# Optimization experiments

Measured on AMD Instinct MI355X. Metric: run time of the kernel, lower is better.

The kernel has to match this reference:

```python
import jax, jax.numpy as jnp
import numpy as np

D_MODEL, D_FF, N_EXPERTS, TOP_K = 1024, 4096, 8, 2
B, S = 2, 2048


def setup_inputs() -> dict:
    key = jax.random.key(0)
    ks = jax.random.split(key, 7)
    scale = 0.02
    return {
        "x": jax.random.normal(ks[0], (B, S, D_MODEL), dtype=jnp.float32),
        "W1": jax.random.normal(ks[1], (N_EXPERTS, D_MODEL, D_FF), dtype=jnp.float32) * scale,
        "b1": jnp.zeros((N_EXPERTS, D_FF), dtype=jnp.float32),
        "W2": jax.random.normal(ks[2], (N_EXPERTS, D_FF, D_MODEL), dtype=jnp.float32) * scale,
        "b2": jnp.zeros((N_EXPERTS, D_MODEL), dtype=jnp.float32),
        "Wg": jax.random.normal(ks[3], (D_MODEL, N_EXPERTS), dtype=jnp.float32) * scale,
        "bg": jnp.zeros((N_EXPERTS,), dtype=jnp.float32),
    }


def reference(x, W1, b1, W2, b2, Wg, bg):
    # x: [B, S, d_model]
    Bx, Sx, d = x.shape
    E = W1.shape[0]
    # Gate + top-k routing (softmax over the top-k scores, as in the torch code)
    logits = jnp.einsum("bsd,de->bse", x, Wg) + bg            # [B,S,E]
    topk_scores, topk_idx = jax.lax.top_k(logits, TOP_K)       # [B,S,K]
    topk_scores = jax.nn.softmax(topk_scores, axis=-1)

    tokens = x.reshape(-1, d)                                  # [T,d]
    idx_flat = topk_idx.reshape(-1, TOP_K)                     # [T,K]
    sc_flat = topk_scores.reshape(-1, TOP_K)                   # [T,K]
    # Per-token combine weight for each expert: sum_k score_k * 1[idx_k == e]
    comb = (jax.nn.one_hot(idx_flat, E, dtype=x.dtype) * sc_flat[..., None]).sum(axis=1)  # [T,E]

    # Dense grouped expert MLP (zero combine weight kills non-selected experts)
    h = jnp.einsum("td,edf->etf", tokens, W1) + b1[:, None, :]  # [E,T,d_ff]
    even = (jnp.arange(E) % 2 == 0)[:, None, None]
    # torch nn.GELU default = exact (erf); odd experts use SiLU
    a = jnp.where(even, jax.nn.gelu(h, approximate=False), jax.nn.silu(h))
    y = jnp.einsum("etf,efd->etd", a, W2) + b2[:, None, :]      # [E,T,d_model]
    out = jnp.einsum("te,etd->td", comb, y)                     # [T,d_model]
    # Dropout is identity in eval mode
    return out.reshape(Bx, Sx, d)
```

## Files before the change

### kernel.cpp

```cpp
#include <hip/hip_runtime.h>
#include <stdint.h>

#define T_TOK 4096
#define DM 1024
#define DF 4096
#define NE 8

typedef __attribute__((ext_vector_type(8))) short bf16x8;
typedef __attribute__((ext_vector_type(4))) float f32x4;

__device__ __forceinline__ float b2f(unsigned short u) {
    union { unsigned int i; float f; } v; v.i = ((unsigned int)u) << 16; return v.f;
}
__device__ __forceinline__ unsigned short f2b(float f) {
    unsigned int i = __float_as_uint(f);
    unsigned int r = (i + 0x7FFFu + ((i >> 16) & 1u)) >> 16;
    return (unsigned short)r;
}
__device__ __forceinline__ void load_lds16(const void* g, void* l) {
    __builtin_amdgcn_global_load_lds((__attribute__((address_space(1))) void*)(g),
                                     (__attribute__((address_space(3))) void*)(l), 16, 0, 0);
}

__device__ __forceinline__ float fexp2(float x) {
#if __has_builtin(__builtin_amdgcn_exp2f)
    return __builtin_amdgcn_exp2f(x);
#else
    return exp2f(x);
#endif
}
__device__ __forceinline__ float frcp(float x) {
#if __has_builtin(__builtin_amdgcn_rcpf)
    return __builtin_amdgcn_rcpf(x);
#else
    return 1.0f / x;
#endif
}

__device__ __forceinline__ float gelu_f(float h) {
    float z = h * 0.70710678118654752f;
    float az = fabsf(z);
    float t = frcp(1.0f + 0.3275911f * az);
    float p = ((((1.061405429f * t - 1.453152027f) * t + 1.421413741f) * t
                - 0.284496736f) * t + 0.254829592f) * t;
    float e = fexp2(-1.4426950408889634f * az * az);
    float er = 1.0f - p * e;
    er = (z < 0.f) ? -er : er;
    return 0.5f * h * (1.0f + er);
}
__device__ __forceinline__ float silu_f(float h) {
    return h * frcp(1.0f + fexp2(-1.4426950408889634f * h));
}

__device__ __forceinline__ int swz_bid(int H) {
    int x = H & 7, k = H >> 3;
    return 8 * x + 64 * (k >> 3) + (k & 7);
}

__global__ __launch_bounds__(256) void detect_kernel(const unsigned short* __restrict__ xu,
                                                     int* __restrict__ flag) {
    const int i = (blockIdx.x * 256 + threadIdx.x) * 4;
    uint2 v = *(const uint2*)&xu[i];
    unsigned int a = v.x, b = v.y;
    int found = 0;
    if (((a >> 7)  & 0xFF) == 0xFF) found = 1;
    if (((a >> 23) & 0xFF) == 0xFF) found = 1;
    if (((b >> 7)  & 0xFF) == 0xFF) found = 1;
    if (((b >> 23) & 0xFF) == 0xFF) found = 1;
    if (__ballot(found) != 0 && (threadIdx.x & 63) == 0) atomicOr(flag, 1);
}

__global__ __launch_bounds__(256) void convx_kernel(const void* __restrict__ xin,
                                                    const int* __restrict__ flag,
                                                    unsigned short* __restrict__ xb) {
    const size_t i = ((size_t)blockIdx.x * 256 + threadIdx.x) * 8;
    if (*flag) {
        const float* xf = (const float*)xin + i;
        float4 a = *(const float4*)xf;
        float4 b = *(const float4*)(xf + 4);
        alignas(16) unsigned short t[8] = { f2b(a.x), f2b(a.y), f2b(a.z), f2b(a.w),
                                            f2b(b.x), f2b(b.y), f2b(b.z), f2b(b.w) };
        *(uint4*)(xb + i) = *(const uint4*)t;
    } else {
        *(uint4*)(xb + i) = *(const uint4*)((const unsigned short*)xin + i);
    }
}

__global__ void convf_kernel(const void* __restrict__ b1, const void* __restrict__ b2,
                             const int* __restrict__ flag,
                             float* __restrict__ d1, float* __restrict__ d2) {
    const int i = blockIdx.x * 256 + threadIdx.x;
    const int isf = *flag;
    if (i < NE * DF) {
        d1[i] = isf ? ((const float*)b1)[i] : b2f(((const unsigned short*)b1)[i]);
    } else {
        int j = i - NE * DF;
        d2[j] = isf ? ((const float*)b2)[j] : b2f(((const unsigned short*)b2)[j]);
    }
}

__global__ __launch_bounds__(256) void transpose_kernel(
    const void* __restrict__ in1, const void* __restrict__ in2,
    unsigned short* __restrict__ out1, unsigned short* __restrict__ out2,
    const int* __restrict__ flag) {
    __shared__ unsigned short tile[64][65];
    const int isf = *flag;
    const void* in; unsigned short* out;
    int R, C, rt, ct; size_t base;
    if (blockIdx.z < 8) {
        in = in1; out = out1; R = DM; C = DF;
        base = (size_t)blockIdx.z * R * C;
        rt = blockIdx.y; ct = blockIdx.x;
    } else {
        in = in2; out = out2; R = DF; C = DM;
        base = (size_t)(blockIdx.z - 8) * R * C;
        ct = blockIdx.x & 15;
        rt = (blockIdx.y << 2) | (blockIdx.x >> 4);
    }
    const int r0 = rt * 64, c0 = ct * 64;
    const int lr = threadIdx.x >> 2;
    const int lc = (threadIdx.x & 3) * 16;
    if (isf) {
        const float* src = (const float*)in + base + (size_t)(r0 + lr) * C + c0 + lc;
#pragma unroll
        for (int q = 0; q < 4; q++) {
            float4 v = *(const float4*)(src + q * 4);
            tile[lr][lc + q * 4 + 0] = f2b(v.x);
            tile[lr][lc + q * 4 + 1] = f2b(v.y);
            tile[lr][lc + q * 4 + 2] = f2b(v.z);
            tile[lr][lc + q * 4 + 3] = f2b(v.w);
        }
    } else {
        const unsigned short* src = (const unsigned short*)in + base + (size_t)(r0 + lr) * C + c0 + lc;
#pragma unroll
        for (int q = 0; q < 2; q++) {
            uint4 v = *(const uint4*)(src + q * 8);
            unsigned int w[4] = { v.x, v.y, v.z, v.w };
#pragma unroll
            for (int j = 0; j < 4; j++) {
                tile[lr][lc + q * 8 + 2 * j]     = (unsigned short)(w[j] & 0xffff);
                tile[lr][lc + q * 8 + 2 * j + 1] = (unsigned short)(w[j] >> 16);
            }
        }
    }
    __syncthreads();
    const int oc = threadIdx.x >> 2;
    const int oj = (threadIdx.x & 3) * 16;
    alignas(16) unsigned short tmp[16];
#pragma unroll
    for (int j = 0; j < 16; j++) tmp[j] = tile[oj + j][oc];
    unsigned short* dst = out + base + (size_t)(c0 + oc) * R + r0 + oj;
    *(uint4*)(dst) = *(const uint4*)(tmp);
    *(uint4*)(dst + 8) = *(const uint4*)(tmp + 8);
}

__global__ __launch_bounds__(256) void gate_kernel(
    const void* __restrict__ x, const void* __restrict__ Wg, const void* __restrict__ bg,
    const int* __restrict__ flag, int* __restrict__ cnt,
    int* __restrict__ tok_e, float* __restrict__ tok_s) {
    const int isf = *flag;
    const int wave = threadIdx.x >> 6, lane = threadIdx.x & 63;
    const int t = blockIdx.x * 4 + wave;
    float p[8] = {0.f,0.f,0.f,0.f,0.f,0.f,0.f,0.f};
    if (isf) {
        const float* xr = (const float*)x + (size_t)t * DM;
        const float* wg = (const float*)Wg;
        for (int i = lane; i < DM; i += 64) {
            float xv = xr[i];
            float4 a = *(const float4*)(wg + (size_t)i * 8);
            float4 b = *(const float4*)(wg + (size_t)i * 8 + 4);
            p[0] += xv * a.x; p[1] += xv * a.y; p[2] += xv * a.z; p[3] += xv * a.w;
            p[4] += xv * b.x; p[5] += xv * b.y; p[6] += xv * b.z; p[7] += xv * b.w;
        }
    } else {
        const unsigned short* xr = (const unsigned short*)x + (size_t)t * DM;
        const unsigned short* wg = (const unsigned short*)Wg;
        for (int i = lane; i < DM; i += 64) {
            float xv = b2f(xr[i]);
            uint4 wv = *(const uint4*)(wg + (size_t)i * 8);
            p[0] += xv * b2f((unsigned short)(wv.x & 0xffff));
            p[1] += xv * b2f((unsigned short)(wv.x >> 16));
            p[2] += xv * b2f((unsigned short)(wv.y & 0xffff));
            p[3] += xv * b2f((unsigned short)(wv.y >> 16));
            p[4] += xv * b2f((unsigned short)(wv.z & 0xffff));
            p[5] += xv * b2f((unsigned short)(wv.z >> 16));
            p[6] += xv * b2f((unsigned short)(wv.w & 0xffff));
            p[7] += xv * b2f((unsigned short)(wv.w >> 16));
        }
    }
    for (int off = 32; off > 0; off >>= 1)
        for (int e = 0; e < 8; e++) p[e] += __shfl_down(p[e], off);
    if (lane == 0) {
        for (int e = 0; e < 8; e++)
            p[e] += isf ? ((const float*)bg)[e] : b2f(((const unsigned short*)bg)[e]);
        int e0 = 0;
        for (int e = 1; e < 8; e++) if (p[e] > p[e0]) e0 = e;
        int e1 = (e0 == 0) ? 1 : 0;
        for (int e = 0; e < 8; e++) if (e != e0 && p[e] > p[e1]) e1 = e;
        float z = expf(p[e1] - p[e0]);
        float s0 = 1.f / (1.f + z);
        tok_e[2 * t] = e0; tok_e[2 * t + 1] = e1;
        tok_s[2 * t] = s0; tok_s[2 * t + 1] = z * s0;
        atomicAdd(&cnt[e0], 1); atomicAdd(&cnt[e1], 1);
    }
}

__global__ void scan_kernel(const int* __restrict__ cnt, int* __restrict__ offs) {
    if (threadIdx.x == 0) {
        int s = 0;
        for (int e = 0; e < NE; e++) { offs[e] = s; s += cnt[e]; }
    }
}

__global__ __launch_bounds__(256) void place_kernel(
    const int* __restrict__ tok_e, const int* __restrict__ offs, int* __restrict__ cnt2,
    int* __restrict__ tok_list, int* __restrict__ slot_of) {
    const int t = blockIdx.x * 256 + threadIdx.x;
    for (int k = 0; k < 2; k++) {
        int e = tok_e[2 * t + k];
        int slot = atomicAdd(&cnt2[e], 1);
        int idx = offs[e] + slot;
        tok_list[idx] = t;
        slot_of[2 * t + k] = idx;
    }
}

__global__ __launch_bounds__(256) void gemm1_kernel(
    const unsigned short* __restrict__ xb, const unsigned short* __restrict__ W1T,
    const float* __restrict__ b1f, const int* __restrict__ tok_list,
    const int* __restrict__ offs, const int* __restrict__ cnt,
    unsigned short* __restrict__ act) {
    const int H = blockIdx.x + 32 * (blockIdx.y + 32 * blockIdx.z);
    const int L = swz_bid(H);
    const int bx = L & 31, by = (L >> 5) & 31, e = L >> 10;
    const int ne = cnt[e];
    if (by * 128 >= ne) return;
    const int off_e = offs[e];
    __shared__ unsigned short Asm[3][128 * 32];
    __shared__ unsigned short Bsm[3][128 * 32];
    __shared__ int toks[128];
    const int tid = threadIdx.x, w = tid >> 6, lane = tid & 63;
    if (tid < 128) {
        int r = by * 128 + tid;
        toks[tid] = tok_list[off_e + (r < ne ? r : ne - 1)];
    }
    __syncthreads();
    const int arow0 = w * 16 + (lane >> 2);
    const int s_sw = (lane >> 3) & 3;
    const int acol = (((lane & 3) ^ s_sw) * 8);
    const int tok0 = toks[arow0], tok1 = toks[arow0 + 64];
    const unsigned short* gA0 = xb + (size_t)tok0 * DM + acol;
    const unsigned short* gA1 = xb + (size_t)tok1 * DM + acol;
    const unsigned short* Wte = W1T + (size_t)e * DF * DM;
    const unsigned short* gB0 = Wte + (size_t)(bx * 128 + arow0) * DM + acol;
    const unsigned short* gB1 = gB0 + (size_t)64 * DM;
    f32x4 acc[4][4] = {};
    const int mb = (w >> 1) * 64, nb = (w & 1) * 64;
    const int rdoff = (((lane >> 4) ^ ((lane >> 1) & 3)) * 8);

#define STAGE1(buf, kk) do { \
        load_lds16(gA0 + (kk), &Asm[buf][(w) * 16 * 32]); \
        load_lds16(gA1 + (kk), &Asm[buf][(w + 4) * 16 * 32]); \
        load_lds16(gB0 + (kk), &Bsm[buf][(w) * 16 * 32]); \
        load_lds16(gB1 + (kk), &Bsm[buf][(w + 4) * 16 * 32]); \
    } while (0)

    STAGE1(0, 0);
    STAGE1(1, 32);
    const int NK = DM / 32;
    int cur = 0, nxt = 2;
    for (int t = 0; t < NK; ++t) {
        if (t + 1 < NK) { asm volatile("s_waitcnt vmcnt(4)" ::: "memory"); }
        else            { asm volatile("s_waitcnt vmcnt(0)" ::: "memory"); }
        __builtin_amdgcn_s_barrier();
        if (t + 2 < NK) STAGE1(nxt, (t + 2) * 32);
        const unsigned short* As = &Asm[cur][0];
        const unsigned short* Bs = &Bsm[cur][0];
        bf16x8 af[4], bfv[4];
#pragma unroll
        for (int i = 0; i < 4; i++)
            af[i] = *(const bf16x8*)&As[(mb + i * 16 + (lane & 15)) * 32 + rdoff];
#pragma unroll
        for (int j = 0; j < 4; j++)
            bfv[j] = *(const bf16x8*)&Bs[(nb + j * 16 + (lane & 15)) * 32 + rdoff];
        __builtin_amdgcn_s_setprio(1);
#pragma unroll
        for (int i = 0; i < 4; i++)
#pragma unroll
            for (int j = 0; j < 4; j++)
                acc[i][j] = __builtin_amdgcn_mfma_f32_16x16x32_bf16(af[i], bfv[j], acc[i][j], 0, 0, 0);
        __builtin_amdgcn_s_setprio(0);
        cur = (cur == 2) ? 0 : cur + 1;
        nxt = (nxt == 2) ? 0 : nxt + 1;
    }
#undef STAGE1

    const bool even_e = (e & 1) == 0;
    const float* b1e = b1f + (size_t)e * DF + bx * 128;
#pragma unroll
    for (int i = 0; i < 4; i++) {
#pragma unroll
        for (int r = 0; r < 4; r++) {
            int m = mb + i * 16 + ((lane >> 4) * 4) + r;
            int grow = by * 128 + m;
            if (grow < ne) {
                unsigned short* dst = act + (size_t)(off_e + grow) * DF + bx * 128;
#pragma unroll
                for (int j = 0; j < 4; j++) {
                    int n = nb + j * 16 + (lane & 15);
                    float h = acc[i][j][r] + b1e[n];
                    float a = even_e ? gelu_f(h) : silu_f(h);
                    dst[n] = f2b(a);
                }
            }
        }
    }
}

__global__ __launch_bounds__(256) void gemm2_kernel(
    const unsigned short* __restrict__ act, const unsigned short* __restrict__ W2T,
    const float* __restrict__ b2f, const int* __restrict__ offs,
    const int* __restrict__ cnt, float* __restrict__ yall) {
    const int H = blockIdx.x + 8 * (blockIdx.y + 32 * blockIdx.z);
    const int L = swz_bid(H);
    const int bx = L & 7, by = (L >> 3) & 31, e = L >> 8;
    const int ne = cnt[e];
    if (by * 128 >= ne) return;
    const int off_e = offs[e];
    __shared__ unsigned short Asm[3][128 * 32];
    __shared__ unsigned short Bsm[3][128 * 32];
    const int tid = threadIdx.x, w = tid >> 6, lane = tid & 63;
    const int arow0 = w * 16 + (lane >> 2);
    const int s_sw = (lane >> 3) & 3;
    const int acol = (((lane & 3) ^ s_sw) * 8);
    int r0 = by * 128 + arow0;       if (r0 > ne - 1) r0 = ne - 1;
    int r1 = by * 128 + arow0 + 64;  if (r1 > ne - 1) r1 = ne - 1;
    const unsigned short* gA0 = act + (size_t)(off_e + r0) * DF + acol;
    const unsigned short* gA1 = act + (size_t)(off_e + r1) * DF + acol;
    const unsigned short* Wte = W2T + (size_t)e * DM * DF;
    const unsigned short* gB0 = Wte + (size_t)(bx * 128 + arow0) * DF + acol;
    const unsigned short* gB1 = gB0 + (size_t)64 * DF;
    f32x4 acc[4][4] = {};
    const int mb = (w >> 1) * 64, nb = (w & 1) * 64;
    const int rdoff = (((lane >> 4) ^ ((lane >> 1) & 3)) * 8);

#define STAGE2(buf, kk) do { \
        load_lds16(gA0 + (kk), &Asm[buf][(w) * 16 * 32]); \
        load_lds16(gA1 + (kk), &Asm[buf][(w + 4) * 16 * 32]); \
        load_lds16(gB0 + (kk), &Bsm[buf][(w) * 16 * 32]); \
        load_lds16(gB1 + (kk), &Bsm[buf][(w + 4) * 16 * 32]); \
    } while (0)

    STAGE2(0, 0);
    STAGE2(1, 32);
    const int NK = DF / 32;
    int cur = 0, nxt = 2;
    for (int t = 0; t < NK; ++t) {
        if (t + 1 < NK) { asm volatile("s_waitcnt vmcnt(4)" ::: "memory"); }
        else            { asm volatile("s_waitcnt vmcnt(0)" ::: "memory"); }
        __builtin_amdgcn_s_barrier();
        if (t + 2 < NK) STAGE2(nxt, (t + 2) * 32);
        const unsigned short* As = &Asm[cur][0];
        const unsigned short* Bs = &Bsm[cur][0];
        bf16x8 af[4], bfv[4];
#pragma unroll
        for (int i = 0; i < 4; i++)
            af[i] = *(const bf16x8*)&As[(mb + i * 16 + (lane & 15)) * 32 + rdoff];
#pragma unroll
        for (int j = 0; j < 4; j++)
            bfv[j] = *(const bf16x8*)&Bs[(nb + j * 16 + (lane & 15)) * 32 + rdoff];
        __builtin_amdgcn_s_setprio(1);
#pragma unroll
        for (int i = 0; i < 4; i++)
#pragma unroll
            for (int j = 0; j < 4; j++)
                acc[i][j] = __builtin_amdgcn_mfma_f32_16x16x32_bf16(af[i], bfv[j], acc[i][j], 0, 0, 0);
        __builtin_amdgcn_s_setprio(0);
        cur = (cur == 2) ? 0 : cur + 1;
        nxt = (nxt == 2) ? 0 : nxt + 1;
    }
#undef STAGE2

    const float* b2e = b2f + (size_t)e * DM + bx * 128;
#pragma unroll
    for (int i = 0; i < 4; i++) {
#pragma unroll
        for (int r = 0; r < 4; r++) {
            int m = mb + i * 16 + ((lane >> 4) * 4) + r;
            int grow = by * 128 + m;
            if (grow < ne) {
                float* dst = yall + (size_t)(off_e + grow) * DM + bx * 128;
#pragma unroll
                for (int j = 0; j < 4; j++) {
                    int n = nb + j * 16 + (lane & 15);
                    dst[n] = acc[i][j][r] + b2e[n];
                }
            }
        }
    }
}

__global__ __launch_bounds__(256) void combine_kernel(
    const float* __restrict__ yall, const int* __restrict__ slot_of,
    const float* __restrict__ tok_s, void* __restrict__ out, const int* __restrict__ flag) {
    const int t = blockIdx.x;
    const int c = threadIdx.x * 4;
    const int s0i = slot_of[2 * t], s1i = slot_of[2 * t + 1];
    const float w0 = tok_s[2 * t], w1 = tok_s[2 * t + 1];
    float4 a = *(const float4*)&yall[(size_t)s0i * DM + c];
    float4 b = *(const float4*)&yall[(size_t)s1i * DM + c];
    float4 r;
    r.x = w0 * a.x + w1 * b.x;
    r.y = w0 * a.y + w1 * b.y;
    r.z = w0 * a.z + w1 * b.z;
    r.w = w0 * a.w + w1 * b.w;
    if (*flag) {
        *(float4*)((float*)out + (size_t)t * DM + c) = r;
    } else {
        ushort4 o;
        o.x = f2b(r.x); o.y = f2b(r.y); o.z = f2b(r.z); o.w = f2b(r.w);
        *(ushort4*)((unsigned short*)out + (size_t)t * DM + c) = o;
    }
}

extern "C" void kernel_launch(void* const* d_in, const int* in_sizes, int n_in,
                              void* d_out, int out_size, void* d_ws, size_t ws_size,
                              hipStream_t stream) {
    (void)in_sizes; (void)n_in; (void)out_size; (void)ws_size;
    const void* x  = d_in[0];
    const void* W1 = d_in[1];
    const void* b1 = d_in[2];
    const void* W2 = d_in[3];
    const void* b2 = d_in[4];
    const void* Wg = d_in[5];
    const void* bg = d_in[6];

    uint8_t* wsb = (uint8_t*)d_ws;
    int* ip = (int*)wsb;
    int* flag  = ip;
    int* cnt   = ip + 8;
    int* cnt2  = ip + 16;
    int* offs  = ip + 24;
    int* tok_e = ip + 32;
    float* tok_s  = (float*)(tok_e + 2 * T_TOK);
    int* tok_list = (int*)(tok_s + 2 * T_TOK);
    int* slot_of  = tok_list + 2 * T_TOK;
    size_t head = (size_t)((uint8_t*)(slot_of + 2 * T_TOK) - wsb);
    head = (head + 255) & ~(size_t)255;
    float* b1f = (float*)(wsb + head);
    float* b2f = b1f + (size_t)NE * DF;
    unsigned short* xb  = (unsigned short*)(b2f + (size_t)NE * DM);
    unsigned short* W1T = xb + (size_t)T_TOK * DM;
    unsigned short* W2T = W1T + (size_t)NE * DM * DF;
    unsigned short* actb = W2T + (size_t)NE * DM * DF;
    float* yall = (float*)W1T;

    hipMemsetAsync(ip, 0, 128, stream);
    detect_kernel<<<256, 256, 0, stream>>>((const unsigned short*)x, flag);
    convx_kernel<<<(T_TOK * DM) / 2048, 256, 0, stream>>>(x, flag, xb);
    convf_kernel<<<(NE * (DF + DM)) / 256, 256, 0, stream>>>(b1, b2, flag, b1f, b2f);
    transpose_kernel<<<dim3(64, 16, 16), 256, 0, stream>>>(W1, W2, W1T, W2T, flag);
    gate_kernel<<<T_TOK / 4, 256, 0, stream>>>(x, Wg, bg, flag, cnt, tok_e, tok_s);
    scan_kernel<<<1, 64, 0, stream>>>(cnt, offs);
    place_kernel<<<T_TOK / 256, 256, 0, stream>>>(tok_e, offs, cnt2, tok_list, slot_of);
    gemm1_kernel<<<dim3(DF / 128, T_TOK / 128, NE), 256, 0, stream>>>(xb, W1T, b1f, tok_list, offs, cnt, actb);
    gemm2_kernel<<<dim3(DM / 128, T_TOK / 128, NE), 256, 0, stream>>>(actb, W2T, b2f, offs, cnt, yall);
    combine_kernel<<<T_TOK, 256, 0, stream>>>(yall, slot_of, tok_s, d_out, flag);
}
```

Before: 757.7 us.

## Deterministic routing compaction, drop block swizzle, manually unroll triple-buffered GEMM loops

Replaces the atomic-based expert counting and placement with a single-block histogram/scan kernel and a per-expert ballot-based stable compaction kernel, making token order deterministic. Removes the block-index swizzle in both grouped GEMMs so blocks map directly to (bx, by, expert). Unrolls the triple-buffered K loops by three with compile-time buffer indices and waitcnt values, removing the runtime buffer rotation and branches. The compaction is serialized per expert across 8K entries with three barriers per step, and dropping the swizzle may change L2 reuse of weight tiles.

New measurement: 715.7 us. 1.06x faster.

```diff
diff --git a/kernel.cpp b/kernel.cpp
--- a/kernel.cpp
+++ b/kernel.cpp
@@ -50,11 +50,6 @@
 }
 __device__ __forceinline__ float silu_f(float h) {
     return h * frcp(1.0f + fexp2(-1.4426950408889634f * h));
-}
-
-__device__ __forceinline__ int swz_bid(int H) {
-    int x = H & 7, k = H >> 3;
-    return 8 * x + 64 * (k >> 3) + (k & 7);
 }
 
 __global__ __launch_bounds__(256) void detect_kernel(const unsigned short* __restrict__ xu,
@@ -156,7 +151,7 @@
 
 __global__ __launch_bounds__(256) void gate_kernel(
     const void* __restrict__ x, const void* __restrict__ Wg, const void* __restrict__ bg,
-    const int* __restrict__ flag, int* __restrict__ cnt,
+    const int* __restrict__ flag,
     int* __restrict__ tok_e, float* __restrict__ tok_s) {
     const int isf = *flag;
     const int wave = threadIdx.x >> 6, lane = threadIdx.x & 63;
@@ -201,27 +196,67 @@
         float s0 = 1.f / (1.f + z);
         tok_e[2 * t] = e0; tok_e[2 * t + 1] = e1;
         tok_s[2 * t] = s0; tok_s[2 * t + 1] = z * s0;
-        atomicAdd(&cnt[e0], 1); atomicAdd(&cnt[e1], 1);
-    }
-}
-
-__global__ void scan_kernel(const int* __restrict__ cnt, int* __restrict__ offs) {
-    if (threadIdx.x == 0) {
+    }
+}
+
+__global__ __launch_bounds__(256) void histscan_kernel(const int* __restrict__ tok_e,
+                                                       int* __restrict__ cnt,
+                                                       int* __restrict__ offs) {
+    const int tid = threadIdx.x, w = tid >> 6, lane = tid & 63;
+    int c[8] = {0,0,0,0,0,0,0,0};
+    for (int i = tid; i < 2 * T_TOK; i += 256) {
+        int v = tok_e[i];
+#pragma unroll
+        for (int e = 0; e < 8; e++) c[e] += (v == e);
+    }
+    for (int off = 32; off > 0; off >>= 1)
+#pragma unroll
+        for (int e = 0; e < 8; e++) c[e] += __shfl_down(c[e], off);
+    __shared__ int ws[4][8];
+    if (lane == 0)
+#pragma unroll
+        for (int e = 0; e < 8; e++) ws[w][e] = c[e];
+    __syncthreads();
+    if (tid == 0) {
         int s = 0;
-        for (int e = 0; e < NE; e++) { offs[e] = s; s += cnt[e]; }
-    }
-}
-
-__global__ __launch_bounds__(256) void place_kernel(
-    const int* __restrict__ tok_e, const int* __restrict__ offs, int* __restrict__ cnt2,
-    int* __restrict__ tok_list, int* __restrict__ slot_of) {
-    const int t = blockIdx.x * 256 + threadIdx.x;
-    for (int k = 0; k < 2; k++) {
-        int e = tok_e[2 * t + k];
-        int slot = atomicAdd(&cnt2[e], 1);
-        int idx = offs[e] + slot;
-        tok_list[idx] = t;
-        slot_of[2 * t + k] = idx;
+        for (int e = 0; e < 8; e++) {
+            int t = ws[0][e] + ws[1][e] + ws[2][e] + ws[3][e];
+            cnt[e] = t; offs[e] = s; s += t;
+        }
+    }
+}
+
+__global__ __launch_bounds__(256) void compact_kernel(const int* __restrict__ tok_e,
+                                                      const int* __restrict__ offs,
+                                                      int* __restrict__ tok_list,
+                                                      int* __restrict__ slot_of) {
+    const int e = blockIdx.x;
+    const int tid = threadIdx.x, w = tid >> 6, lane = tid & 63;
+    __shared__ int wtot[4];
+    __shared__ int running;
+    if (tid == 0) running = 0;
+    __syncthreads();
+    const int base = offs[e];
+    for (int i0 = 0; i0 < 2 * T_TOK; i0 += 256) {
+        const int i = i0 + tid;
+        const int v = tok_e[i];
+        const bool pred = (v == e);
+        unsigned long long m = __ballot(pred);
+        int rank = __popcll(m & ((1ull << lane) - 1ull));
+        if (lane == 0) wtot[w] = __popcll(m);
+        __syncthreads();
+        int woff = 0;
+        for (int ww = 0; ww < w; ww++) woff += wtot[ww];
+        const int tot = wtot[0] + wtot[1] + wtot[2] + wtot[3];
+        const int r = running;
+        if (pred) {
+            int pos = base + r + woff + rank;
+            tok_list[pos] = i >> 1;
+            slot_of[i] = pos;
+        }
+        __syncthreads();
+        if (tid == 0) running += tot;
+        __syncthreads();
     }
 }
 
@@ -230,9 +265,7 @@
     const float* __restrict__ b1f, const int* __restrict__ tok_list,
     const int* __restrict__ offs, const int* __restrict__ cnt,
     unsigned short* __restrict__ act) {
-    const int H = blockIdx.x + 32 * (blockIdx.y + 32 * blockIdx.z);
-    const int L = swz_bid(H);
-    const int bx = L & 31, by = (L >> 5) & 31, e = L >> 10;
+    const int e = blockIdx.z, by = blockIdx.y, bx = blockIdx.x;
     const int ne = cnt[e];
     if (by * 128 >= ne) return;
     const int off_e = offs[e];
@@ -265,34 +298,37 @@
         load_lds16(gB1 + (kk), &Bsm[buf][(w + 4) * 16 * 32]); \
     } while (0)
 
+#define GBODY1(W, DOSTAGE, p, s, kk) do { \
+        asm volatile("s_waitcnt vmcnt(" #W ")" ::: "memory"); \
+        __builtin_amdgcn_s_barrier(); \
+        if (DOSTAGE) { STAGE1(s, kk); } \
+        bf16x8 af[4], bfv[4]; \
+        _Pragma("unroll") \
+        for (int i = 0; i < 4; i++) \
+            af[i] = *(const bf16x8*)&Asm[p][(mb + i * 16 + (lane & 15)) * 32 + rdoff]; \
+        _Pragma("unroll") \
+        for (int j = 0; j < 4; j++) \
+            bfv[j] = *(const bf16x8*)&Bsm[p][(nb + j * 16 + (lane & 15)) * 32 + rdoff]; \
+        __builtin_amdgcn_s_setprio(1); \
+        _Pragma("unroll") \
+        for (int i = 0; i < 4; i++) \
+            _Pragma("unroll") \
+            for (int j = 0; j < 4; j++) \
+                acc[i][j] = __builtin_amdgcn_mfma_f32_16x16x32_bf16(af[i], bfv[j], acc[i][j], 0, 0, 0); \
+        __builtin_amdgcn_s_setprio(0); \
+    } while (0)
+
     STAGE1(0, 0);
     STAGE1(1, 32);
-    const int NK = DM / 32;
-    int cur = 0, nxt = 2;
-    for (int t = 0; t < NK; ++t) {
-        if (t + 1 < NK) { asm volatile("s_waitcnt vmcnt(4)" ::: "memory"); }
-        else            { asm volatile("s_waitcnt vmcnt(0)" ::: "memory"); }
-        __builtin_amdgcn_s_barrier();
-        if (t + 2 < NK) STAGE1(nxt, (t + 2) * 32);
-        const unsigned short* As = &Asm[cur][0];
-        const unsigned short* Bs = &Bsm[cur][0];
-        bf16x8 af[4], bfv[4];
-#pragma unroll
-        for (int i = 0; i < 4; i++)
-            af[i] = *(const bf16x8*)&As[(mb + i * 16 + (lane & 15)) * 32 + rdoff];
-#pragma unroll
-        for (int j = 0; j < 4; j++)
-            bfv[j] = *(const bf16x8*)&Bs[(nb + j * 16 + (lane & 15)) * 32 + rdoff];
-        __builtin_amdgcn_s_setprio(1);
-#pragma unroll
-        for (int i = 0; i < 4; i++)
-#pragma unroll
-            for (int j = 0; j < 4; j++)
-                acc[i][j] = __builtin_amdgcn_mfma_f32_16x16x32_bf16(af[i], bfv[j], acc[i][j], 0, 0, 0);
-        __builtin_amdgcn_s_setprio(0);
-        cur = (cur == 2) ? 0 : cur + 1;
-        nxt = (nxt == 2) ? 0 : nxt + 1;
-    }
+    for (int t3 = 0; t3 < 30; t3 += 3) {
+        const int kb = t3 * 32;
+        GBODY1(4, true, 0, 2, kb + 64);
+        GBODY1(4, true, 1, 0, kb + 96);
+        GBODY1(4, true, 2, 1, kb + 128);
+    }
+    GBODY1(4, false, 0, 0, 0);
+    GBODY1(0, false, 1, 0, 0);
+#undef GBODY1
 #undef STAGE1
 
     const bool even_e = (e & 1) == 0;
@@ -321,9 +357,7 @@
     const unsigned short* __restrict__ act, const unsigned short* __restrict__ W2T,
     const float* __restrict__ b2f, const int* __restrict__ offs,
     const int* __restrict__ cnt, float* __restrict__ yall) {
-    const int H = blockIdx.x + 8 * (blockIdx.y + 32 * blockIdx.z);
-    const int L = swz_bid(H);
-    const int bx = L & 7, by = (L >> 3) & 31, e = L >> 8;
+    const int e = blockIdx.z, by = blockIdx.y, bx = blockIdx.x;
     const int ne = cnt[e];
     if (by * 128 >= ne) return;
     const int off_e = offs[e];
@@ -351,34 +385,37 @@
         load_lds16(gB1 + (kk), &Bsm[buf][(w + 4) * 16 * 32]); \
     } while (0)
 
+#define GBODY2(W, DOSTAGE, p, s, kk) do { \
+        asm volatile("s_waitcnt vmcnt(" #W ")" ::: "memory"); \
+        __builtin_amdgcn_s_barrier(); \
+        if (DOSTAGE) { STAGE2(s, kk); } \
+        bf16x8 af[4], bfv[4]; \
+        _Pragma("unroll") \
+        for (int i = 0; i < 4; i++) \
+            af[i] = *(const bf16x8*)&Asm[p][(mb + i * 16 + (lane & 15)) * 32 + rdoff]; \
+        _Pragma("unroll") \
+        for (int j = 0; j < 4; j++) \
+            bfv[j] = *(const bf16x8*)&Bsm[p][(nb + j * 16 + (lane & 15)) * 32 + rdoff]; \
+        __builtin_amdgcn_s_setprio(1); \
+        _Pragma("unroll") \
+        for (int i = 0; i < 4; i++) \
+            _Pragma("unroll") \
+            for (int j = 0; j < 4; j++) \
+                acc[i][j] = __builtin_amdgcn_mfma_f32_16x16x32_bf16(af[i], bfv[j], acc[i][j], 0, 0, 0); \
+        __builtin_amdgcn_s_setprio(0); \
+    } while (0)
+
     STAGE2(0, 0);
     STAGE2(1, 32);
-    const int NK = DF / 32;
-    int cur = 0, nxt = 2;
-    for (int t = 0; t < NK; ++t) {
-        if (t + 1 < NK) { asm volatile("s_waitcnt vmcnt(4)" ::: "memory"); }
-        else            { asm volatile("s_waitcnt vmcnt(0)" ::: "memory"); }
-        __builtin_amdgcn_s_barrier();
-        if (t + 2 < NK) STAGE2(nxt, (t + 2) * 32);
-        const unsigned short* As = &Asm[cur][0];
-        const unsigned short* Bs = &Bsm[cur][0];
-        bf16x8 af[4], bfv[4];
-#pragma unroll
-        for (int i = 0; i < 4; i++)
-            af[i] = *(const bf16x8*)&As[(mb + i * 16 + (lane & 15)) * 32 + rdoff];
-#pragma unroll
-        for (int j = 0; j < 4; j++)
-            bfv[j] = *(const bf16x8*)&Bs[(nb + j * 16 + (lane & 15)) * 32 + rdoff];
-        __builtin_amdgcn_s_setprio(1);
-#pragma unroll
-        for (int i = 0; i < 4; i++)
-#pragma unroll
-            for (int j = 0; j < 4; j++)
-                acc[i][j] = __builtin_amdgcn_mfma_f32_16x16x32_bf16(af[i], bfv[j], acc[i][j], 0, 0, 0);
-        __builtin_amdgcn_s_setprio(0);
-        cur = (cur == 2) ? 0 : cur + 1;
-        nxt = (nxt == 2) ? 0 : nxt + 1;
-    }
+    for (int t3 = 0; t3 < 126; t3 += 3) {
+        const int kb = t3 * 32;
+        GBODY2(4, true, 0, 2, kb + 64);
+        GBODY2(4, true, 1, 0, kb + 96);
+        GBODY2(4, true, 2, 1, kb + 128);
+    }
+    GBODY2(4, false, 0, 0, 0);
+    GBODY2(0, false, 1, 0, 0);
+#undef GBODY2
 #undef STAGE2
 
     const float* b2e = b2f + (size_t)e * DM + bx * 128;
@@ -454,15 +491,16 @@
     unsigned short* W2T = W1T + (size_t)NE * DM * DF;
     unsigned short* actb = W2T + (size_t)NE * DM * DF;
     float* yall = (float*)W1T;
+    (void)cnt2;
 
     hipMemsetAsync(ip, 0, 128, stream);
     detect_kernel<<<256, 256, 0, stream>>>((const unsigned short*)x, flag);
     convx_kernel<<<(T_TOK * DM) / 2048, 256, 0, stream>>>(x, flag, xb);
     convf_kernel<<<(NE * (DF + DM)) / 256, 256, 0, stream>>>(b1, b2, flag, b1f, b2f);
     transpose_kernel<<<dim3(64, 16, 16), 256, 0, stream>>>(W1, W2, W1T, W2T, flag);
-    gate_kernel<<<T_TOK / 4, 256, 0, stream>>>(x, Wg, bg, flag, cnt, tok_e, tok_s);
-    scan_kernel<<<1, 64, 0, stream>>>(cnt, offs);
-    place_kernel<<<T_TOK / 256, 256, 0, stream>>>(tok_e, offs, cnt2, tok_list, slot_of);
+    gate_kernel<<<T_TOK / 4, 256, 0, stream>>>(x, Wg, bg, flag, tok_e, tok_s);
+    histscan_kernel<<<1, 256, 0, stream>>>(tok_e, cnt, offs);
+    compact_kernel<<<NE, 256, 0, stream>>>(tok_e, offs, tok_list, slot_of);
     gemm1_kernel<<<dim3(DF / 128, T_TOK / 128, NE), 256, 0, stream>>>(xb, W1T, b1f, tok_list, offs, cnt, actb);
     gemm2_kernel<<<dim3(DM / 128, T_TOK / 128, NE), 256, 0, stream>>>(actb, W2T, b2f, offs, cnt, yall);
     combine_kernel<<<T_TOK, 256, 0, stream>>>(yall, slot_of, tok_s, d_out, flag);
```
